# Kernel optimization log

Hardware: AMD Instinct MI355X
Metric: run time of the kernel (lower is better)

## Reference

```python
import jax, jax.numpy as jnp
import numpy as np

N = 100000   # nodes
E = 1600000  # edges
IN, H, OUT = 128, 128, 40
BN_EPS = 1e-5


def setup_inputs() -> dict:
    key = jax.random.key(0)
    ks = jax.random.split(key, 8)
    x = jax.random.normal(ks[0], (N, IN), jnp.float32)
    edge_src = jax.random.randint(ks[1], (E,), 0, N, jnp.int32)
    edge_dst = jax.random.randint(ks[2], (E,), 0, N, jnp.int32)

    def glorot(k, shape):
        lim = (6.0 / (shape[0] + shape[1])) ** 0.5
        return jax.random.uniform(k, shape, jnp.float32, -lim, lim)

    return {
        "x": x, "edge_src": edge_src, "edge_dst": edge_dst,
        "W1": glorot(ks[3], (IN, H)), "b1": jnp.zeros((H,), jnp.float32),
        "g1": jnp.ones((H,), jnp.float32), "bt1": jnp.zeros((H,), jnp.float32),
        "W2": glorot(ks[4], (H, H)), "b2": jnp.zeros((H,), jnp.float32),
        "g2": jnp.ones((H,), jnp.float32), "bt2": jnp.zeros((H,), jnp.float32),
        "Wr": glorot(ks[5], (H, OUT)), "br": jnp.zeros((OUT,), jnp.float32),
    }


def _gcn_conv(h_in, W, b, src, dst, dinv):
    # GCNConv: D^{-1/2}(A+I)D^{-1/2} X W + b  (symmetric norm w/ self-loops)
    h = h_in @ W                                   # [N,H]
    coef = dinv[src] * dinv[dst]                   # [E]
    agg = jax.ops.segment_sum(h[src] * coef[:, None], dst, num_segments=N)
    agg = agg + h * (dinv * dinv)[:, None]         # self-loop contribution
    return agg + b


def _bn_relu(h, gamma, beta):
    # BatchNorm1d in training mode (batch stats, biased variance) + ReLU
    mean = jnp.mean(h, axis=0)
    var = jnp.var(h, axis=0)
    y = (h - mean) * jax.lax.rsqrt(var + BN_EPS) * gamma + beta
    return jax.nn.relu(y)


def reference(x, edge_src, edge_dst, W1, b1, g1, bt1, W2, b2, g2, bt2, Wr, br):
    ones = jnp.ones((E,), jnp.float32)
    deg = jax.ops.segment_sum(ones, edge_dst, num_segments=N) + 1.0  # +1 self-loop
    dinv = jax.lax.rsqrt(deg)

    h = _gcn_conv(x, W1, b1, edge_src, edge_dst, dinv)
    h = _bn_relu(h, g1, bt1)
    h = _gcn_conv(h, W2, b2, edge_src, edge_dst, dinv)
    h = _bn_relu(h, g2, bt2)
    # dropout omitted (deterministic eval); readout linear
    return h @ Wr + br
```

## Files before the change

### kernel.cpp

```cpp
#include <hip/hip_runtime.h>
#include <hip/hip_bf16.h>
#include <hip/hip_fp16.h>

#define H_DIM 128

typedef _Float16 half8 __attribute__((ext_vector_type(8)));
typedef float floatx4 __attribute__((ext_vector_type(4)));

__device__ inline int imax(int a, int b) { return a > b ? a : b; }

__global__ void degree_kernel(const int* __restrict__ dst, int* __restrict__ deg, int E_) {
    int i = blockIdx.x * blockDim.x + threadIdx.x;
    if (i < E_) atomicAdd(&deg[dst[i]], 1);
}

__global__ void scan_block_kernel(const int* __restrict__ deg, float* __restrict__ dinv,
                                  int* __restrict__ rowptr, int* __restrict__ bsum, int N_) {
    __shared__ int sh[256];
    int i = blockIdx.x * 256 + threadIdx.x;
    int v = (i < N_) ? deg[i] : 0;
    if (i < N_) dinv[i] = rsqrtf((float)v + 1.0f);
    int pd = (i < N_) ? imax(24, (v + 7) & ~7) : 0;
    sh[threadIdx.x] = pd;
    __syncthreads();
    for (int off = 1; off < 256; off <<= 1) {
        int t = (threadIdx.x >= off) ? sh[threadIdx.x - off] : 0;
        __syncthreads();
        sh[threadIdx.x] += t;
        __syncthreads();
    }
    if (i < N_) rowptr[i] = sh[threadIdx.x] - pd;
    if (threadIdx.x == 255) bsum[blockIdx.x] = sh[255];
}

__global__ void scan_add_kernel(int* __restrict__ rowptr, const int* __restrict__ bsum,
                                const int* __restrict__ deg, int* __restrict__ cols, int N_) {
    __shared__ int red[256];
    const int b = blockIdx.x, t = threadIdx.x;
    int s = 0;
    for (int j = t; j < b; j += 256) s += bsum[j];
    red[t] = s;
    __syncthreads();
    for (int off = 128; off > 0; off >>= 1) {
        if (t < off) red[t] += red[t + off];
        __syncthreads();
    }
    int boff = red[0];
    int i = b * 256 + t;
    if (i < N_) {
        int start = rowptr[i] + boff;
        rowptr[i] = start;
        int d = deg[i];
        int pd = imax(24, (d + 7) & ~7);
        int padv = N_ << 8;
        for (int j = start + d; j < start + pd; ++j) cols[j] = padv;
        if (i == N_ - 1) rowptr[N_] = start + pd;
    }
}

__global__ void csr_fill_kernel(const int* __restrict__ src, const int* __restrict__ dst,
                                const int* __restrict__ rowptr, int* __restrict__ cursor,
                                int* __restrict__ cols, int E_, int N_, int shift) {
    int b = blockIdx.x & 7;
    if (((N_ - 1) >> shift) < b) return;
    int i = (blockIdx.x >> 3) * blockDim.x + threadIdx.x;
    if (i < E_) {
        int d = dst[i];
        if ((d >> shift) == b) {
            int p = rowptr[d] + atomicAdd(&cursor[d], 1);
            cols[p] = src[i] << 8;
        }
    }
}

__device__ inline half8 a_frag_f32(const float* Xr, int k0) {
    float4 v0 = *(const float4*)(Xr + k0);
    float4 v1 = *(const float4*)(Xr + k0 + 4);
    half8 a;
    a[0] = (_Float16)v0.x; a[1] = (_Float16)v0.y; a[2] = (_Float16)v0.z; a[3] = (_Float16)v0.w;
    a[4] = (_Float16)v1.x; a[5] = (_Float16)v1.y; a[6] = (_Float16)v1.z; a[7] = (_Float16)v1.w;
    return a;
}
__device__ inline half8 a_frag_f16_bn(const _Float16* Xr, int k0,
                                      const float* A, const float* B) {
    half8 r = *(const half8*)(Xr + k0);
    float4 a0 = *(const float4*)(A + k0);
    float4 a1 = *(const float4*)(A + k0 + 4);
    float4 b0 = *(const float4*)(B + k0);
    float4 b1 = *(const float4*)(B + k0 + 4);
    half8 o;
    o[0] = (_Float16)fmaxf(fmaf((float)r[0], a0.x, b0.x), 0.f);
    o[1] = (_Float16)fmaxf(fmaf((float)r[1], a0.y, b0.y), 0.f);
    o[2] = (_Float16)fmaxf(fmaf((float)r[2], a0.z, b0.z), 0.f);
    o[3] = (_Float16)fmaxf(fmaf((float)r[3], a0.w, b0.w), 0.f);
    o[4] = (_Float16)fmaxf(fmaf((float)r[4], a1.x, b1.x), 0.f);
    o[5] = (_Float16)fmaxf(fmaf((float)r[5], a1.y, b1.y), 0.f);
    o[6] = (_Float16)fmaxf(fmaf((float)r[6], a1.z, b1.z), 0.f);
    o[7] = (_Float16)fmaxf(fmaf((float)r[7], a1.w, b1.w), 0.f);
    return o;
}

template<bool BN, typename InT>
__global__ __launch_bounds__(256) void gemm_mfma_kernel(
    const InT* __restrict__ X, const float* __restrict__ W,
    const float* __restrict__ gsum, const float* __restrict__ gsq,
    const float* __restrict__ gamma, const float* __restrict__ beta,
    const float* __restrict__ dinv,
    _Float16* __restrict__ Y, int N_)
{
    __shared__ _Float16 Wf[32 * 64 * 8];
    __shared__ __align__(16) float Alds[128], Blds[128];

    const int tid = threadIdx.x;
    if constexpr (BN) {
        if (tid < 128) {
            float inv_n = 1.0f / (float)N_;
            float mean = gsum[tid] * inv_n;
            float var  = gsq[tid] * inv_n - mean * mean;
            float a = rsqrtf(var + 1e-5f) * gamma[tid];
            Alds[tid] = a;
            Blds[tid] = beta[tid] - mean * a;
        }
    }
    for (int idx = tid; idx < 128 * 32; idx += 256) {
        int k = idx >> 5;
        int n0 = (idx & 31) * 4;
        float4 w = *(const float4*)(W + k * 128 + n0);
        int kb = k >> 5, q = (k >> 3) & 3, j = k & 7;
#pragma unroll
        for (int u = 0; u < 4; ++u) {
            int n = n0 + u;
            int lane = (n & 15) | (q << 4);
            Wf[((((n >> 4) * 4 + kb) * 64 + lane) << 3) + j] = (_Float16)((&w.x)[u]);
        }
    }
    __syncthreads();

    const int wv = tid >> 6, lane = tid & 63;
    const int m = lane & 15, q = lane >> 4;
    const int row0 = blockIdx.x * 64 + wv * 16;

    int arow = row0 + m;
    if (arow >= N_) arow = N_ - 1;
    const InT* Xr = X + (size_t)arow * H_DIM;

    half8 a[4];
#pragma unroll
    for (int kb = 0; kb < 4; ++kb) {
        int k0 = kb * 32 + q * 8;
        if constexpr (BN) a[kb] = a_frag_f16_bn((const _Float16*)Xr, k0, Alds, Blds);
        else              a[kb] = a_frag_f32((const float*)Xr, k0);
    }

    floatx4 acc[8];
#pragma unroll
    for (int nt = 0; nt < 8; ++nt) acc[nt] = (floatx4){0.f, 0.f, 0.f, 0.f};

#pragma unroll
    for (int nt = 0; nt < 8; ++nt) {
#pragma unroll
        for (int kb = 0; kb < 4; ++kb) {
            half8 b = *(const half8*)&Wf[(((nt * 4 + kb) * 64 + lane) << 3)];
            acc[nt] = __builtin_amdgcn_mfma_f32_16x16x32_f16(a[kb], b, acc[nt], 0, 0, 0);
        }
    }

#pragma unroll
    for (int r = 0; r < 4; ++r) {
        int row = row0 + q * 4 + r;
        if (row < N_) {
            float ds = dinv[row];
            _Float16* Yr = Y + (size_t)row * H_DIM + m;
#pragma unroll
            for (int nt = 0; nt < 8; ++nt)
                Yr[nt * 16] = (_Float16)(ds * acc[nt][r]);
        }
    }
}

__global__ __launch_bounds__(256) void readout_mfma_kernel(
    const _Float16* __restrict__ X, const float* __restrict__ W,
    const float* __restrict__ gsum, const float* __restrict__ gsq,
    const float* __restrict__ gamma, const float* __restrict__ beta,
    const float* __restrict__ br,
    float* __restrict__ Y, int N_, int OUTC)
{
    __shared__ _Float16 Wf[12 * 64 * 8];
    __shared__ __align__(16) float Alds[128], Blds[128];

    const int tid = threadIdx.x;
    if (tid < 128) {
        float inv_n = 1.0f / (float)N_;
        float mean = gsum[tid] * inv_n;
        float var  = gsq[tid] * inv_n - mean * mean;
        float a = rsqrtf(var + 1e-5f) * gamma[tid];
        Alds[tid] = a;
        Blds[tid] = beta[tid] - mean * a;
    }
    for (int idx = tid; idx < 128 * 64; idx += 256) {
        int k = idx >> 6, n = idx & 63;
        if (n < 48) {
            float w = (n < OUTC) ? W[k * OUTC + n] : 0.f;
            int kb = k >> 5, q = (k >> 3) & 3, j = k & 7;
            int lane = (n & 15) | (q << 4);
            Wf[((((n >> 4) * 4 + kb) * 64 + lane) << 3) + j] = (_Float16)w;
        }
    }
    __syncthreads();

    const int wv = tid >> 6, lane = tid & 63;
    const int m = lane & 15, q = lane >> 4;
    const int row0 = blockIdx.x * 64 + wv * 16;

    int arow = row0 + m;
    if (arow >= N_) arow = N_ - 1;
    const _Float16* Xr = X + (size_t)arow * H_DIM;

    half8 a[4];
#pragma unroll
    for (int kb = 0; kb < 4; ++kb)
        a[kb] = a_frag_f16_bn(Xr, kb * 32 + q * 8, Alds, Blds);

    floatx4 acc[3];
#pragma unroll
    for (int nt = 0; nt < 3; ++nt) acc[nt] = (floatx4){0.f, 0.f, 0.f, 0.f};

#pragma unroll
    for (int nt = 0; nt < 3; ++nt) {
#pragma unroll
        for (int kb = 0; kb < 4; ++kb) {
            half8 b = *(const half8*)&Wf[(((nt * 4 + kb) * 64 + lane) << 3)];
            acc[nt] = __builtin_amdgcn_mfma_f32_16x16x32_f16(a[kb], b, acc[nt], 0, 0, 0);
        }
    }

#pragma unroll
    for (int nt = 0; nt < 3; ++nt) {
        int col = nt * 16 + m;
        if (col < OUTC) {
            float bb = br[col];
#pragma unroll
            for (int r = 0; r < 4; ++r) {
                int row = row0 + q * 4 + r;
                if (row < N_)
                    Y[(size_t)row * OUTC + col] = acc[nt][r] + bb;
            }
        }
    }
}

__global__ __launch_bounds__(256) void aggregate_stats_kernel(
    const __half2* __restrict__ Gp,
    const int* __restrict__ rowptr,
    const int* __restrict__ cols,
    const float* __restrict__ dinv, const float* __restrict__ bias,
    __half2* __restrict__ out,
    float* __restrict__ gsum, float* __restrict__ gsq,
    int N_, int stride)
{
    const int wave = threadIdx.x >> 6;
    const int lane = threadIdx.x & 63;
    const int c2 = lane * 2;
    const float bs0 = bias[c2], bs1 = bias[c2 + 1];
    const char* gpb = (const char*)Gp;
    const unsigned lane4 = (unsigned)lane * 4u;
    const __half2 z = __float2half2_rn(0.f);

    float r0 = 0.f, r1 = 0.f, q0 = 0.f, q1 = 0.f;

    const int n0 = blockIdx.x * 4 + wave;
    int e0 = 0, e1 = 0, f0 = 0, f1 = 0;
    int c[24];
    if (n0 < N_) {
        e0 = __builtin_amdgcn_readfirstlane(rowptr[n0]);
        e1 = __builtin_amdgcn_readfirstlane(rowptr[n0 + 1]);
        int n1 = n0 + stride; if (n1 > N_ - 1) n1 = N_ - 1;
        f0 = __builtin_amdgcn_readfirstlane(rowptr[n1]);
        f1 = __builtin_amdgcn_readfirstlane(rowptr[n1 + 1]);
#pragma unroll
        for (int u = 0; u < 24; ++u) c[u] = cols[e0 + u];
    }

    for (int n = n0; n < N_; n += stride) {
        __half2 self = *(const __half2*)(gpb + (((unsigned)n << 8) + lane4));
        __half2 h[24];
#pragma unroll
        for (int u = 0; u < 24; ++u)
            h[u] = *(const __half2*)(gpb + ((unsigned)c[u] + lane4));

        int n2 = n + 2 * stride; if (n2 > N_ - 1) n2 = N_ - 1;
        int g0 = __builtin_amdgcn_readfirstlane(rowptr[n2]);
        int g1 = __builtin_amdgcn_readfirstlane(rowptr[n2 + 1]);

#pragma unroll
        for (int u = 0; u < 24; ++u) c[u] = cols[f0 + u];

        __half2 acc[8];
        acc[0] = self;
#pragma unroll
        for (int u = 1; u < 8; ++u) acc[u] = z;
#pragma unroll
        for (int u = 0; u < 24; ++u)
            acc[u & 7] = __hadd2(acc[u & 7], h[u]);

        for (int e = e0 + 24; e < e1; e += 8) {
            __half2 t[8];
#pragma unroll
            for (int u = 0; u < 8; ++u)
                t[u] = *(const __half2*)(gpb + ((unsigned)cols[e + u] + lane4));
#pragma unroll
            for (int u = 0; u < 8; ++u) acc[u] = __hadd2(acc[u], t[u]);
        }

        __half2 p0 = __hadd2(__hadd2(acc[0], acc[1]), __hadd2(acc[2], acc[3]));
        __half2 p1 = __hadd2(__hadd2(acc[4], acc[5]), __hadd2(acc[6], acc[7]));
        float2 F0 = __half22float2(p0);
        float2 F1 = __half22float2(p1);
        float di = dinv[n];
        float o0 = fmaf(di, F0.x + F1.x, bs0);
        float o1 = fmaf(di, F0.y + F1.y, bs1);
        out[((size_t)n << 6) + lane] = __floats2half2_rn(o0, o1);

        r0 += o0; r1 += o1;
        q0 = fmaf(o0, o0, q0); q1 = fmaf(o1, o1, q1);

        e0 = f0; e1 = f1; f0 = g0; f1 = g1;
    }

    __shared__ float ssum[4][128], ssq[4][128];
    ssum[wave][c2] = r0; ssum[wave][c2 + 1] = r1;
    ssq[wave][c2]  = q0; ssq[wave][c2 + 1]  = q1;
    __syncthreads();
    if (threadIdx.x < 128) {
        int k = threadIdx.x;
        float s = (ssum[0][k] + ssum[1][k]) + (ssum[2][k] + ssum[3][k]);
        float q = (ssq[0][k] + ssq[1][k]) + (ssq[2][k] + ssq[3][k]);
        atomicAdd(&gsum[k], s);
        atomicAdd(&gsq[k], q);
    }
}

extern "C" void kernel_launch(void* const* d_in, const int* in_sizes, int n_in,
                              void* d_out, int out_size, void* d_ws, size_t ws_size,
                              hipStream_t stream) {
    const float* x   = (const float*)d_in[0];
    const int* esrc  = (const int*)d_in[1];
    const int* edst  = (const int*)d_in[2];
    const float* W1  = (const float*)d_in[3];
    const float* b1  = (const float*)d_in[4];
    const float* g1  = (const float*)d_in[5];
    const float* bt1 = (const float*)d_in[6];
    const float* W2  = (const float*)d_in[7];
    const float* b2  = (const float*)d_in[8];
    const float* g2  = (const float*)d_in[9];
    const float* bt2 = (const float*)d_in[10];
    const float* Wr  = (const float*)d_in[11];
    const float* br  = (const float*)d_in[12];

    const int N_ = in_sizes[0] / H_DIM;
    const int E_ = in_sizes[1];
    const int OUTC = out_size / N_;

    char* p = (char*)d_ws;
    auto alloc = [&](size_t bytes) -> void* {
        void* r = (void*)p;
        p += (bytes + 255) & ~(size_t)255;
        return r;
    };
    __half* tmpA = (__half*)alloc((size_t)(N_ + 1) * H_DIM * 2);
    __half* tmpB = (__half*)alloc((size_t)(N_ + 1) * H_DIM * 2);
    int*   cols  = (int*)  alloc(((size_t)E_ + 31 * (size_t)N_ + 64) * 4);
    int*   rowptr= (int*)  alloc((size_t)(N_ + 1) * 4);
    size_t degcur_sz = ((size_t)2 * N_ * 4 + 255) & ~(size_t)255;
    int*   degcur= (int*)  alloc((size_t)2 * N_ * 4);
    float* bnbuf = (float*)alloc(8 * 128 * 4);
    int*   deg   = degcur;
    int*   cursor= degcur + N_;
    float* sum1 = bnbuf,       *sq1 = bnbuf + 128;
    float* sum2 = bnbuf + 256, *sq2 = bnbuf + 384;
    float* dinv  = (float*)alloc((size_t)N_ * 4);
    int*   bsum  = (int*)  alloc(4096);

    hipMemsetAsync(degcur, 0, degcur_sz + 4 * 128 * 4, stream);
    hipMemsetAsync(tmpA + (size_t)N_ * H_DIM, 0, H_DIM * 2, stream);
    hipMemsetAsync(tmpB + (size_t)N_ * H_DIM, 0, H_DIM * 2, stream);

    const int nb = (N_ + 255) / 256;
    const int eb = (E_ + 255) / 256;
    const int ntiles64 = (N_ + 63) / 64;

    int shift = 0;
    while (((N_ - 1) >> shift) > 7) ++shift;

    const int AGG_BLOCKS = 2048;
    const int AGG_STRIDE = AGG_BLOCKS * 4;

    degree_kernel<<<eb, 256, 0, stream>>>(edst, deg, E_);
    scan_block_kernel<<<nb, 256, 0, stream>>>(deg, dinv, rowptr, bsum, N_);
    scan_add_kernel<<<nb, 256, 0, stream>>>(rowptr, bsum, deg, cols, N_);
    csr_fill_kernel<<<eb * 8, 256, 0, stream>>>(esrc, edst, rowptr, cursor, cols, E_, N_, shift);

    gemm_mfma_kernel<false, float><<<ntiles64, 256, 0, stream>>>(
        x, W1, nullptr, nullptr, nullptr, nullptr, dinv, (_Float16*)tmpA, N_);
    aggregate_stats_kernel<<<AGG_BLOCKS, 256, 0, stream>>>(
        (const __half2*)tmpA, rowptr, cols, dinv, b1, (__half2*)tmpB,
        sum1, sq1, N_, AGG_STRIDE);

    gemm_mfma_kernel<true, _Float16><<<ntiles64, 256, 0, stream>>>(
        (const _Float16*)tmpB, W2, sum1, sq1, g1, bt1, dinv, (_Float16*)tmpA, N_);
    aggregate_stats_kernel<<<AGG_BLOCKS, 256, 0, stream>>>(
        (const __half2*)tmpA, rowptr, cols, dinv, b2, (__half2*)tmpB,
        sum2, sq2, N_, AGG_STRIDE);

    readout_mfma_kernel<<<ntiles64, 256, 0, stream>>>(
        (const _Float16*)tmpB, Wr, sum2, sq2, g2, bt2, br, (float*)d_out, N_, OUTC);
}
```

Before: 509.2 us.

## Double-buffer neighbor feature gathers across nodes and shrink row padding to 16

```diff
diff --git a/kernel.cpp b/kernel.cpp
--- a/kernel.cpp
+++ b/kernel.cpp
@@ -8,6 +8,7 @@
 typedef float floatx4 __attribute__((ext_vector_type(4)));
 
 __device__ inline int imax(int a, int b) { return a > b ? a : b; }
+__device__ inline int imin(int a, int b) { return a < b ? a : b; }
 
 __global__ void degree_kernel(const int* __restrict__ dst, int* __restrict__ deg, int E_) {
     int i = blockIdx.x * blockDim.x + threadIdx.x;
@@ -20,7 +21,7 @@
     int i = blockIdx.x * 256 + threadIdx.x;
     int v = (i < N_) ? deg[i] : 0;
     if (i < N_) dinv[i] = rsqrtf((float)v + 1.0f);
-    int pd = (i < N_) ? imax(24, (v + 7) & ~7) : 0;
+    int pd = (i < N_) ? imax(16, (v + 7) & ~7) : 0;
     sh[threadIdx.x] = pd;
     __syncthreads();
     for (int off = 1; off < 256; off <<= 1) {
@@ -51,7 +52,7 @@
         int start = rowptr[i] + boff;
         rowptr[i] = start;
         int d = deg[i];
-        int pd = imax(24, (d + 7) & ~7);
+        int pd = imax(16, (d + 7) & ~7);
         int padv = N_ << 8;
         for (int j = start + d; j < start + pd; ++j) cols[j] = padv;
         if (i == N_ - 1) rowptr[N_] = start + pd;
@@ -249,6 +250,45 @@
     }
 }
 
+#define PHASE(HCUR, CNXT, HNXT, E0, E1, EN0, EN1)                                   \
+    {                                                                               \
+        int nNN = imin(n + 2 * stride, N_ - 1);                                     \
+        int t0 = __builtin_amdgcn_readfirstlane(rowptr[nNN]);                       \
+        int t1 = __builtin_amdgcn_readfirstlane(rowptr[nNN + 1]);                   \
+        _Pragma("unroll")                                                           \
+        for (int u = 0; u < 16; ++u)        \
+            HNXT[u] = *(const __half2*)(gpb + ((unsigned)CNXT[u] + lane4));         \
+        __half2 self = *(const __half2*)(gpb + (((unsigned)n << 8) + lane4));       \
+        _Pragma("unroll")                                                           \
+        for (int u = 0; u < 16; ++u)   \
+            CNXT[u] = cols[t0 + u];                                                 \
+        __half2 acc[8];                                                             \
+        acc[0] = self;                                                              \
+        _Pragma("unroll")                                                           \
+        for (int u = 1; u < 8; ++u) acc[u] = z;                                     \
+        _Pragma("unroll")                                                           \
+        for (int u = 0; u < 16; ++u) acc[u & 7] = __hadd2(acc[u & 7], HCUR[u]);     \
+        for (int e = E0 + 16; e < E1; e += 8) {    \
+            __half2 tt[8];                                                          \
+            _Pragma("unroll")                                                       \
+            for (int u = 0; u < 8; ++u)                                             \
+                tt[u] = *(const __half2*)(gpb + ((unsigned)cols[e + u] + lane4));   \
+            _Pragma("unroll")                                                       \
+            for (int u = 0; u < 8; ++u) acc[u] = __hadd2(acc[u], tt[u]);            \
+        }                                                                           \
+        __half2 p0 = __hadd2(__hadd2(acc[0], acc[1]), __hadd2(acc[2], acc[3]));     \
+        __half2 p1 = __hadd2(__hadd2(acc[4], acc[5]), __hadd2(acc[6], acc[7]));     \
+        float2 F0 = __half22float2(p0);                                             \
+        float2 F1 = __half22float2(p1);                                             \
+        float di = dinv[n];                                                         \
+        float o0 = fmaf(di, F0.x + F1.x, bs0);                                      \
+        float o1 = fmaf(di, F0.y + F1.y, bs1);                                      \
+        out[((size_t)n << 6) + lane] = __floats2half2_rn(o0, o1);                   \
+        r0 += o0; r1 += o1;                                                         \
+        q0 = fmaf(o0, o0, q0); q1 = fmaf(o1, o1, q1);                               \
+        E0 = EN0; E1 = EN1; EN0 = t0; EN1 = t1;                  \
+    }
+
 __global__ __launch_bounds__(256) void aggregate_stats_kernel(
     const __half2* __restrict__ Gp,
     const int* __restrict__ rowptr,
@@ -268,63 +308,32 @@
 
     float r0 = 0.f, r1 = 0.f, q0 = 0.f, q1 = 0.f;
 
-    const int n0 = blockIdx.x * 4 + wave;
-    int e0 = 0, e1 = 0, f0 = 0, f1 = 0;
-    int c[24];
-    if (n0 < N_) {
-        e0 = __builtin_amdgcn_readfirstlane(rowptr[n0]);
-        e1 = __builtin_amdgcn_readfirstlane(rowptr[n0 + 1]);
-        int n1 = n0 + stride; if (n1 > N_ - 1) n1 = N_ - 1;
-        f0 = __builtin_amdgcn_readfirstlane(rowptr[n1]);
-        f1 = __builtin_amdgcn_readfirstlane(rowptr[n1 + 1]);
-#pragma unroll
-        for (int u = 0; u < 24; ++u) c[u] = cols[e0 + u];
-    }
-
-    for (int n = n0; n < N_; n += stride) {
-        __half2 self = *(const __half2*)(gpb + (((unsigned)n << 8) + lane4));
-        __half2 h[24];
-#pragma unroll
-        for (int u = 0; u < 24; ++u)
-            h[u] = *(const __half2*)(gpb + ((unsigned)c[u] + lane4));
-
-        int n2 = n + 2 * stride; if (n2 > N_ - 1) n2 = N_ - 1;
-        int g0 = __builtin_amdgcn_readfirstlane(rowptr[n2]);
-        int g1 = __builtin_amdgcn_readfirstlane(rowptr[n2 + 1]);
-
-#pragma unroll
-        for (int u = 0; u < 24; ++u) c[u] = cols[f0 + u];
-
-        __half2 acc[8];
-        acc[0] = self;
-#pragma unroll
-        for (int u = 1; u < 8; ++u) acc[u] = z;
-#pragma unroll
-        for (int u = 0; u < 24; ++u)
-            acc[u & 7] = __hadd2(acc[u & 7], h[u]);
-
-        for (int e = e0 + 24; e < e1; e += 8) {
-            __half2 t[8];
-#pragma unroll
-            for (int u = 0; u < 8; ++u)
-                t[u] = *(const __half2*)(gpb + ((unsigned)cols[e + u] + lane4));
-#pragma unroll
-            for (int u = 0; u < 8; ++u) acc[u] = __hadd2(acc[u], t[u]);
-        }
-
-        __half2 p0 = __hadd2(__hadd2(acc[0], acc[1]), __hadd2(acc[2], acc[3]));
-        __half2 p1 = __hadd2(__hadd2(acc[4], acc[5]), __hadd2(acc[6], acc[7]));
-        float2 F0 = __half22float2(p0);
-        float2 F1 = __half22float2(p1);
-        float di = dinv[n];
-        float o0 = fmaf(di, F0.x + F1.x, bs0);
-        float o1 = fmaf(di, F0.y + F1.y, bs1);
-        out[((size_t)n << 6) + lane] = __floats2half2_rn(o0, o1);
-
-        r0 += o0; r1 += o1;
-        q0 = fmaf(o0, o0, q0); q1 = fmaf(o1, o1, q1);
-
-        e0 = f0; e1 = f1; f0 = g0; f1 = g1;
+    const int gw = blockIdx.x * 4 + wave;
+    int cX[16], cY[16];
+    __half2 hX[16], hY[16];
+    int eA0 = __builtin_amdgcn_readfirstlane(rowptr[gw]);
+    int eA1 = __builtin_amdgcn_readfirstlane(rowptr[gw + 1]);
+    {
+        int nB = imin(gw + stride, N_ - 1);
+        int b0 = __builtin_amdgcn_readfirstlane(rowptr[nB]);
+        int b1 = __builtin_amdgcn_readfirstlane(rowptr[nB + 1]);
+#pragma unroll
+        for (int u = 0; u < 16; ++u) cX[u] = cols[eA0 + u];
+#pragma unroll
+        for (int u = 0; u < 16; ++u)
+            hX[u] = *(const __half2*)(gpb + ((unsigned)cX[u] + lane4));
+#pragma unroll
+        for (int u = 0; u < 16; ++u) cX[u] = cols[b0 + u];
+        int eB0 = b0, eB1 = b1;
+        int n = gw;
+        while (true) {
+            PHASE(hX, cX, hY, eA0, eA1, eB0, eB1)
+            n += stride;
+            if (n >= N_) break;
+            PHASE(hY, cX, hX, eA0, eA1, eB0, eB1)
+            n += stride;
+            if (n >= N_) break;
+        }
     }
 
     __shared__ float ssum[4][128], ssq[4][128];
```

New measurement: 516.8 us. No clear change (+1.5%).

## Double-buffer neighbor gathers in aggregation kernel to prefetch next node's rows

Applied to the files above, without the earlier changes.

```diff
diff --git a/kernel.cpp b/kernel.cpp
--- a/kernel.cpp
+++ b/kernel.cpp
@@ -8,6 +8,7 @@
 typedef float floatx4 __attribute__((ext_vector_type(4)));
 
 __device__ inline int imax(int a, int b) { return a > b ? a : b; }
+__device__ inline int imin(int a, int b) { return a < b ? a : b; }
 
 __global__ void degree_kernel(const int* __restrict__ dst, int* __restrict__ deg, int E_) {
     int i = blockIdx.x * blockDim.x + threadIdx.x;
@@ -249,6 +250,48 @@
     }
 }
 
+#define RF(x) __builtin_amdgcn_readfirstlane(x)
+
+#define PHASE(HCUR, HNXT)                                                          \
+    {                                                                              \
+        __builtin_amdgcn_sched_barrier(0);                                         \
+        _Pragma("unroll")                                                          \
+        for (int u = 0; u < 24; ++u)                \
+            HNXT[u] = *(const __half2*)(gpb + ((unsigned)cN[u] + lane4));          \
+        __half2 self = *(const __half2*)(gpb + (((unsigned)n << 8) + lane4));      \
+        __builtin_amdgcn_sched_barrier(0);                                         \
+        int n2 = imin(n + 2 * stride, N_ - 1);                                     \
+        int t0 = RF(rowptr[n2]);                                                   \
+        int t1 = RF(rowptr[n2 + 1]);                                               \
+        _Pragma("unroll")                                                          \
+        for (int u = 0; u < 24; ++u) cN[u] = cols[t0 + u];     \
+        __half2 acc[8];                                                            \
+        acc[0] = self;                                                             \
+        _Pragma("unroll")                                                          \
+        for (int u = 1; u < 8; ++u) acc[u] = z;                                    \
+        _Pragma("unroll")                                                          \
+        for (int u = 0; u < 24; ++u) acc[u & 7] = __hadd2(acc[u & 7], HCUR[u]);    \
+        for (int e = eC0 + 24; e < eC1; e += 8) {  \
+            __half2 tt[8];                                                         \
+            _Pragma("unroll")                                                      \
+            for (int u = 0; u < 8; ++u)                                            \
+                tt[u] = *(const __half2*)(gpb + ((unsigned)cols[e + u] + lane4));  \
+            _Pragma("unroll")                                                      \
+            for (int u = 0; u < 8; ++u) acc[u] = __hadd2(acc[u], tt[u]);           \
+        }                                                                          \
+        __half2 p0 = __hadd2(__hadd2(acc[0], acc[1]), __hadd2(acc[2], acc[3]));    \
+        __half2 p1 = __hadd2(__hadd2(acc[4], acc[5]), __hadd2(acc[6], acc[7]));    \
+        float2 F0 = __half22float2(p0);                                            \
+        float2 F1 = __half22float2(p1);                                            \
+        float di = dinv[n];                                                        \
+        float o0 = fmaf(di, F0.x + F1.x, bs0);                                     \
+        float o1 = fmaf(di, F0.y + F1.y, bs1);                                     \
+        out[((size_t)n << 6) + lane] = __floats2half2_rn(o0, o1);                  \
+        r0 += o0; r1 += o1;                                                        \
+        q0 = fmaf(o0, o0, q0); q1 = fmaf(o1, o1, q1);                              \
+        eC0 = eN0; eC1 = eN1; eN0 = t0; eN1 = t1;               \
+    }
+
 __global__ __launch_bounds__(256) void aggregate_stats_kernel(
     const __half2* __restrict__ Gp,
     const int* __restrict__ rowptr,
@@ -268,63 +311,34 @@
 
     float r0 = 0.f, r1 = 0.f, q0 = 0.f, q1 = 0.f;
 
-    const int n0 = blockIdx.x * 4 + wave;
-    int e0 = 0, e1 = 0, f0 = 0, f1 = 0;
-    int c[24];
-    if (n0 < N_) {
-        e0 = __builtin_amdgcn_readfirstlane(rowptr[n0]);
-        e1 = __builtin_amdgcn_readfirstlane(rowptr[n0 + 1]);
-        int n1 = n0 + stride; if (n1 > N_ - 1) n1 = N_ - 1;
-        f0 = __builtin_amdgcn_readfirstlane(rowptr[n1]);
-        f1 = __builtin_amdgcn_readfirstlane(rowptr[n1 + 1]);
-#pragma unroll
-        for (int u = 0; u < 24; ++u) c[u] = cols[e0 + u];
-    }
-
-    for (int n = n0; n < N_; n += stride) {
-        __half2 self = *(const __half2*)(gpb + (((unsigned)n << 8) + lane4));
-        __half2 h[24];
+    const int gw = blockIdx.x * 4 + wave;
+    int eC0 = RF(rowptr[gw]);
+    int eC1 = RF(rowptr[gw + 1]);
+    int nB = imin(gw + stride, N_ - 1);
+    int eN0 = RF(rowptr[nB]);
+    int eN1 = RF(rowptr[nB + 1]);
+
+    __half2 hA[24], hB[24];
+    int cN[24];
+    {
+        int cC[24];
+#pragma unroll
+        for (int u = 0; u < 24; ++u) cC[u] = cols[eC0 + u];
 #pragma unroll
         for (int u = 0; u < 24; ++u)
-            h[u] = *(const __half2*)(gpb + ((unsigned)c[u] + lane4));
-
-        int n2 = n + 2 * stride; if (n2 > N_ - 1) n2 = N_ - 1;
-        int g0 = __builtin_amdgcn_readfirstlane(rowptr[n2]);
-        int g1 = __builtin_amdgcn_readfirstlane(rowptr[n2 + 1]);
-
-#pragma unroll
-        for (int u = 0; u < 24; ++u) c[u] = cols[f0 + u];
-
-        __half2 acc[8];
-        acc[0] = self;
-#pragma unroll
-        for (int u = 1; u < 8; ++u) acc[u] = z;
-#pragma unroll
-        for (int u = 0; u < 24; ++u)
-            acc[u & 7] = __hadd2(acc[u & 7], h[u]);
-
-        for (int e = e0 + 24; e < e1; e += 8) {
-            __half2 t[8];
-#pragma unroll
-            for (int u = 0; u < 8; ++u)
-                t[u] = *(const __half2*)(gpb + ((unsigned)cols[e + u] + lane4));
-#pragma unroll
-            for (int u = 0; u < 8; ++u) acc[u] = __hadd2(acc[u], t[u]);
-        }
-
-        __half2 p0 = __hadd2(__hadd2(acc[0], acc[1]), __hadd2(acc[2], acc[3]));
-        __half2 p1 = __hadd2(__hadd2(acc[4], acc[5]), __hadd2(acc[6], acc[7]));
-        float2 F0 = __half22float2(p0);
-        float2 F1 = __half22float2(p1);
-        float di = dinv[n];
-        float o0 = fmaf(di, F0.x + F1.x, bs0);
-        float o1 = fmaf(di, F0.y + F1.y, bs1);
-        out[((size_t)n << 6) + lane] = __floats2half2_rn(o0, o1);
-
-        r0 += o0; r1 += o1;
-        q0 = fmaf(o0, o0, q0); q1 = fmaf(o1, o1, q1);
-
-        e0 = f0; e1 = f1; f0 = g0; f1 = g1;
+            hA[u] = *(const __half2*)(gpb + ((unsigned)cC[u] + lane4));
+    }
+#pragma unroll
+    for (int u = 0; u < 24; ++u) cN[u] = cols[eN0 + u];
+
+    int n = gw;
+    while (true) {
+        PHASE(hA, hB)
+        n += stride;
+        if (n >= N_) break;
+        PHASE(hB, hA)
+        n += stride;
+        if (n >= N_) break;
     }
 
     __shared__ float ssum[4][128], ssq[4][128];
```

After: 517.7 us. Within noise of the previous version (+1.7%).
